# Kernel tuning notes

Measured on AMD Instinct MI355X. Metric: run time of the kernel, lower is better.

The kernel has to match this reference:

```python
import jax, jax.numpy as jnp
import numpy as np

NUM_LAYERS = 4  # -> 9 blocks: 4 encoder + bottleneck + 4 decoder
EPS = 1e-6
SQRT2 = float(np.sqrt(2.0))
INV_SQRT3 = float(1.0 / np.sqrt(3.0))


def _block(s, v, W0, W1, Wa, Wb):
    """_SelfInteractionUNet with full_square=False, irreps = Mx0e + Mx1o.

    tensor_square of per-channel (0e+1o):
      0e: s*s ; 0e: |v|^2/sqrt(3) ; 1o: sqrt(2)*s*v ; (2e is produced by e3nn
      but irreps_out has no 2e so the Linear discards it -> omitted here).
    """
    M = s.shape[-1]
    ts0a = s * s                                    # [N, M] 0e
    ts0b = jnp.sum(v * v, axis=-1) * INV_SQRT3      # [N, M] 0e
    ts1 = SQRT2 * s[..., None] * v                  # [N, M, 3] 1o
    s_in = jnp.concatenate([s, ts0a, ts0b], axis=-1)   # [N, 3M]
    v_in = jnp.concatenate([v, ts1], axis=1)           # [N, 2M, 3]
    # irreps-segmented Linear with path (fan-in) normalization
    s2 = (s_in @ W0) * (1.0 / np.sqrt(s_in.shape[-1]))               # [N, Mo]
    v2 = jnp.einsum('ncd,co->nod', v_in, W1) * (1.0 / np.sqrt(v_in.shape[1]))  # [N, Mo, 3]
    Mo = W0.shape[-1]
    # gated MLP on invariants (0e part), silu after each layer
    h = jax.nn.silu((s2 @ Wa) * (1.0 / np.sqrt(Mo)))                 # [N, Mo]
    g = jax.nn.silu((h @ Wb) * (1.0 / np.sqrt(Mo)))                  # [N, 2Mo]
    s2 = s2 * g[:, :Mo]
    v2 = v2 * g[:, Mo:, None]
    return s2, v2


def _eq_layernorm(s, v):
    # scalars: center + RMS normalize; vectors: norm-RMS normalize (equivariant)
    s = s - jnp.mean(s, axis=-1, keepdims=True)
    s = s * jax.lax.rsqrt(jnp.mean(s * s, axis=-1, keepdims=True) + EPS)
    v = v * jax.lax.rsqrt(jnp.mean(v * v, axis=(1, 2), keepdims=True) + EPS)
    return s, v


def _unet(scalars, vectors, W0, W1, Wa, Wb):
    s, v = scalars, vectors
    skips = []
    for i in range(NUM_LAYERS):
        s, v = _block(s, v, W0[i], W1[i], Wa[i], Wb[i])
        s, v = _eq_layernorm(s, v)
        skips.append((s, v))
    s, v = _block(s, v, W0[NUM_LAYERS], W1[NUM_LAYERS], Wa[NUM_LAYERS], Wb[NUM_LAYERS])
    for j in range(NUM_LAYERS):
        ss, vs = skips[NUM_LAYERS - 1 - j]
        s, v = s + ss, v + vs
        k = NUM_LAYERS + 1 + j
        s, v = _block(s, v, W0[k], W1[k], Wa[k], Wb[k])
        if j < NUM_LAYERS - 1:  # no norm on last decoder layer (norm_last=False)
            s, v = _eq_layernorm(s, v)
    N = s.shape[0]
    return jnp.concatenate([s, v.reshape(N, -1)], axis=-1)  # [N, 4M] irreps_array layout


def setup_inputs() -> dict:
    key = jax.random.key(0)
    ks = jax.random.split(key, 6)
    N, M = 16384, 256
    return {
        'scalars': jax.random.normal(ks[0], (N, M), jnp.float32),
        'vectors': jax.random.normal(ks[1], (N, M, 3), jnp.float32),
        'W0': jax.random.normal(ks[2], (9, 3 * M, M), jnp.float32),
        'W1': jax.random.normal(ks[3], (9, 2 * M, M), jnp.float32),
        'Wa': jax.random.normal(ks[4], (9, M, M), jnp.float32),
        'Wb': jax.random.normal(ks[5], (9, M, 2 * M), jnp.float32),
    }


def reference(scalars, vectors, W0, W1, Wa, Wb):
    return _unet(scalars, vectors, W0, W1, Wa, Wb)
```

## Files before the change

kernel.cpp:

```cpp
#include <hip/hip_runtime.h>
#include <hip/hip_bf16.h>
#include <math.h>


typedef __attribute__((ext_vector_type(8))) short bf16x8;
typedef __attribute__((ext_vector_type(4))) short bf16x4;
typedef __attribute__((ext_vector_type(4))) float f32x4;
typedef __attribute__((ext_vector_type(4))) _Float16 f16x4;

__device__ __forceinline__ unsigned asu(float f){ union{float f;unsigned u;}x; x.f=f; return x.u; }
__device__ __forceinline__ float asf(unsigned u){ union{unsigned u;float f;}x; x.u=u; return x.f; }

__device__ __forceinline__ unsigned short f2bf_r(float f){
  unsigned i = asu(f);
  return (unsigned short)((i + 0x7fffu + ((i >> 16) & 1u)) >> 16);
}
__device__ __forceinline__ float bf2f(unsigned short u){ return asf(((unsigned)u) << 16); }

__device__ __forceinline__ void split_t(float f, short& hi, short& lo){
  unsigned u = asu(f);
  hi = (short)(u >> 16);
  float lof = f - asf(u & 0xffff0000u);
  lo = (short)(asu(lof) >> 16);
}
__device__ __forceinline__ float rec(short h, short l){
  return asf(((unsigned)(unsigned short)h) << 16) + asf(((unsigned)(unsigned short)l) << 16);
}
__device__ __forceinline__ f32x4 rec4(const unsigned short* H, const unsigned short* L, size_t o){
  bf16x4 hv = *(const bf16x4*)(H + o);
  bf16x4 lv = *(const bf16x4*)(L + o);
  f32x4 f;
  #pragma unroll
  for (int j = 0; j < 4; ++j) f[j] = rec(hv[j], lv[j]);
  return f;
}

__global__ __launch_bounds__(256)
void transpose_w(const float* __restrict__ W, unsigned short* __restrict__ Wh,
                 unsigned short* __restrict__ Wl, int K, int Mo){
  __shared__ float tile[32][33];
  const int bi = blockIdx.z;
  const float* Wb = W + (size_t)bi * K * Mo;
  const size_t wo = (size_t)bi * K * Mo;
  const int k0 = blockIdx.x * 32, o0 = blockIdx.y * 32;
  const int tx = threadIdx.x & 31, ty = threadIdx.x >> 5;
  #pragma unroll
  for (int i = 0; i < 4; ++i){
    int k = ty + i * 8;
    tile[k][tx] = Wb[(size_t)(k0 + k) * Mo + o0 + tx];
  }
  __syncthreads();
  #pragma unroll
  for (int i = 0; i < 4; ++i){
    int o = ty + i * 8;
    float f = tile[tx][o];
    unsigned short h = f2bf_r(f);
    unsigned short l = f2bf_r(f - bf2f(h));
    Wh[wo + (size_t)(o0 + o) * K + k0 + tx] = h;
    Wl[wo + (size_t)(o0 + o) * K + k0 + tx] = l;
  }
}

__global__ __launch_bounds__(256)
void convert_inputs(const float* __restrict__ s, const float* __restrict__ v,
                    unsigned short* __restrict__ stH, unsigned short* __restrict__ stL,
                    int NM){
  int i = blockIdx.x * 256 + threadIdx.x;
  if (i >= NM) return;
  short h, l;
  split_t(s[i], h, l); stH[i] = h; stL[i] = l;
  const float* vp = v + (size_t)i * 3;
  #pragma unroll
  for (int d = 0; d < 3; ++d){
    split_t(vp[d], h, l);
    stH[(size_t)(1 + d) * NM + i] = h;
    stL[(size_t)(1 + d) * NM + i] = l;
  }
}

__global__ __launch_bounds__(256, 3)
void gemm_sv(const unsigned short* __restrict__ StH, const unsigned short* __restrict__ StL,
             const _Float16* __restrict__ skip,
             const unsigned short* __restrict__ W0h, const unsigned short* __restrict__ W0l,
             const unsigned short* __restrict__ W1h, const unsigned short* __restrict__ W1l,
             unsigned short* __restrict__ s2H, unsigned short* __restrict__ s2L,
             unsigned short* __restrict__ v2H, unsigned short* __restrict__ v2L,
             int NM, float cs, float cv)
{
  __shared__ unsigned short Ah[32][40], Al[32][40];
  __shared__ unsigned short Bhs[256][40], Bls[256][40];
  const int tid  = threadIdx.x;
  const int lane = tid & 63;
  const int wave = tid >> 6;
  const int wn   = wave * 64;
  const int row0 = blockIdx.x * 32;
  const int z    = blockIdx.z;
  const bool isS = (z == 0);
  const int dv   = z - 1;
  const int K    = isS ? 768 : 512;
  const float scale = isS ? cs : cv;
  const unsigned short* Bh = isS ? W0h : W1h;
  const unsigned short* Bl = isS ? W0l : W1l;
  unsigned short* outH = isS ? s2H : v2H + (size_t)dv * NM;
  unsigned short* outL = isS ? s2L : v2L + (size_t)dv * NM;
  const bool sk = (skip != nullptr);

  f32x4 acc[2][4];
  #pragma unroll
  for (int m = 0; m < 2; ++m)
    #pragma unroll
    for (int n = 0; n < 4; ++n) acc[m][n] = (f32x4){0.f,0.f,0.f,0.f};

  const int ar = tid >> 3;
  const int ac4 = (tid & 7) * 4;

  for (int k0 = 0; k0 < K; k0 += 32){
    const int seg = k0 >> 8;
    {
      const int gr = row0 + ar;
      const int c  = (k0 + ac4) & 255;
      const size_t o = (size_t)gr * 256 + c;
      if (!sk && seg == 0){
        const int p = isS ? 0 : 1 + dv;
        *(bf16x4*)(&Ah[ar][ac4]) = *(const bf16x4*)(StH + (size_t)p * NM + o);
        *(bf16x4*)(&Al[ar][ac4]) = *(const bf16x4*)(StL + (size_t)p * NM + o);
      } else {
        f32x4 f;
        if (isS){
          if (seg <= 1){
            f32x4 x = rec4(StH, StL, o);
            if (sk){
              f16x4 y = *(const f16x4*)(skip + o);
              #pragma unroll
              for (int j = 0; j < 4; ++j) x[j] += (float)y[j];
            }
            if (seg == 0){
              f = x;
            } else {
              #pragma unroll
              for (int j = 0; j < 4; ++j) f[j] = x[j]*x[j];
            }
          } else {
            f32x4 a0 = rec4(StH, StL, (size_t)NM + o);
            f32x4 a1 = rec4(StH, StL, (size_t)2*NM + o);
            f32x4 a2 = rec4(StH, StL, (size_t)3*NM + o);
            if (sk){
              f16x4 b0 = *(const f16x4*)(skip + (size_t)NM + o);
              f16x4 b1 = *(const f16x4*)(skip + (size_t)2*NM + o);
              f16x4 b2 = *(const f16x4*)(skip + (size_t)3*NM + o);
              #pragma unroll
              for (int j = 0; j < 4; ++j){ a0[j]+=(float)b0[j]; a1[j]+=(float)b1[j]; a2[j]+=(float)b2[j]; }
            }
            #pragma unroll
            for (int j = 0; j < 4; ++j)
              f[j] = (a0[j]*a0[j] + a1[j]*a1[j] + a2[j]*a2[j]) * 0.57735026918962576f;
          }
        } else {
          f32x4 x = rec4(StH, StL, (size_t)(1+dv)*NM + o);
          if (sk){
            f16x4 y = *(const f16x4*)(skip + (size_t)(1+dv)*NM + o);
            #pragma unroll
            for (int j = 0; j < 4; ++j) x[j] += (float)y[j];
          }
          if (seg == 0){
            f = x;
          } else {
            f32x4 s = rec4(StH, StL, o);
            if (sk){
              f16x4 y = *(const f16x4*)(skip + o);
              #pragma unroll
              for (int j = 0; j < 4; ++j) s[j] += (float)y[j];
            }
            #pragma unroll
            for (int j = 0; j < 4; ++j) f[j] = 1.41421356237309505f * s[j] * x[j];
          }
        }
        bf16x4 hi, lo;
        #pragma unroll
        for (int j = 0; j < 4; ++j){ short h, l; split_t(f[j], h, l); hi[j]=h; lo[j]=l; }
        *(bf16x4*)(&Ah[ar][ac4]) = hi;
        *(bf16x4*)(&Al[ar][ac4]) = lo;
      }
    }
    #pragma unroll
    for (int it = 0; it < 4; ++it){
      int idx = tid + it * 256;
      int br  = idx >> 2;
      int kc  = (idx & 3) * 8;
      const size_t o = (size_t)br * K + k0 + kc;
      *(bf16x8*)(&Bhs[br][kc]) = *(const bf16x8*)(Bh + o);
      *(bf16x8*)(&Bls[br][kc]) = *(const bf16x8*)(Bl + o);
    }
    __syncthreads();

    const int arow = lane & 15;
    const int kq   = (lane >> 4) * 8;
    bf16x8 ah[2], al[2], bh[4], bl[4];
    #pragma unroll
    for (int m = 0; m < 2; ++m){
      ah[m] = *(const bf16x8*)(&Ah[m*16 + arow][kq]);
      al[m] = *(const bf16x8*)(&Al[m*16 + arow][kq]);
    }
    #pragma unroll
    for (int n = 0; n < 4; ++n){
      bh[n] = *(const bf16x8*)(&Bhs[wn + n*16 + arow][kq]);
      bl[n] = *(const bf16x8*)(&Bls[wn + n*16 + arow][kq]);
    }
    #pragma unroll
    for (int m = 0; m < 2; ++m)
      #pragma unroll
      for (int n = 0; n < 4; ++n){
        acc[m][n] = __builtin_amdgcn_mfma_f32_16x16x32_bf16(ah[m], bh[n], acc[m][n], 0, 0, 0);
        acc[m][n] = __builtin_amdgcn_mfma_f32_16x16x32_bf16(al[m], bh[n], acc[m][n], 0, 0, 0);
        acc[m][n] = __builtin_amdgcn_mfma_f32_16x16x32_bf16(ah[m], bl[n], acc[m][n], 0, 0, 0);
      }
    __syncthreads();
  }

  #pragma unroll
  for (int m = 0; m < 2; ++m){
    #pragma unroll
    for (int n = 0; n < 4; ++n){
      const int cg = wn + n * 16 + (lane & 15);
      #pragma unroll
      for (int j = 0; j < 4; ++j){
        const int rg = row0 + m * 16 + ((lane >> 4) * 4) + j;
        short h, l; split_t(acc[m][n][j] * scale, h, l);
        outH[(size_t)rg * 256 + cg] = (unsigned short)h;
        outL[(size_t)rg * 256 + cg] = (unsigned short)l;
      }
    }
  }
}

template<int EPI>
__global__ __launch_bounds__(256, 3)
void gemm_hg(const unsigned short* __restrict__ AhG, const unsigned short* __restrict__ AlG,
             const unsigned short* __restrict__ Bh, const unsigned short* __restrict__ Bl,
             int NM, float scale,
             unsigned short* __restrict__ outH, unsigned short* __restrict__ outL,
             const unsigned short* __restrict__ s2H, const unsigned short* __restrict__ s2L,
             const unsigned short* __restrict__ v2H, const unsigned short* __restrict__ v2L,
             unsigned short* __restrict__ stH, unsigned short* __restrict__ stL,
             float* __restrict__ fout)
{
  __shared__ unsigned short Ah[32][40], Al[32][40];
  __shared__ unsigned short Bhs[256][40], Bls[256][40];
  const int tid  = threadIdx.x;
  const int lane = tid & 63;
  const int wave = tid >> 6;
  const int wn   = wave * 64;
  const int row0 = blockIdx.x * 32;
  const int col0 = blockIdx.y * 256;
  const int K = 256;

  f32x4 acc[2][4];
  #pragma unroll
  for (int m = 0; m < 2; ++m)
    #pragma unroll
    for (int n = 0; n < 4; ++n) acc[m][n] = (f32x4){0.f,0.f,0.f,0.f};

  const int ar = tid >> 3;
  const int ac4 = (tid & 7) * 4;

  for (int k0 = 0; k0 < K; k0 += 32){
    {
      const size_t o = (size_t)(row0 + ar) * 256 + k0 + ac4;
      *(bf16x4*)(&Ah[ar][ac4]) = *(const bf16x4*)(AhG + o);
      *(bf16x4*)(&Al[ar][ac4]) = *(const bf16x4*)(AlG + o);
    }
    #pragma unroll
    for (int it = 0; it < 4; ++it){
      int idx = tid + it * 256;
      int br  = idx >> 2;
      int kc  = (idx & 3) * 8;
      const size_t o = (size_t)(col0 + br) * K + k0 + kc;
      *(bf16x8*)(&Bhs[br][kc]) = *(const bf16x8*)(Bh + o);
      *(bf16x8*)(&Bls[br][kc]) = *(const bf16x8*)(Bl + o);
    }
    __syncthreads();

    const int arow = lane & 15;
    const int kq   = (lane >> 4) * 8;
    bf16x8 ah[2], al[2], bh[4], bl[4];
    #pragma unroll
    for (int m = 0; m < 2; ++m){
      ah[m] = *(const bf16x8*)(&Ah[m*16 + arow][kq]);
      al[m] = *(const bf16x8*)(&Al[m*16 + arow][kq]);
    }
    #pragma unroll
    for (int n = 0; n < 4; ++n){
      bh[n] = *(const bf16x8*)(&Bhs[wn + n*16 + arow][kq]);
      bl[n] = *(const bf16x8*)(&Bls[wn + n*16 + arow][kq]);
    }
    #pragma unroll
    for (int m = 0; m < 2; ++m)
      #pragma unroll
      for (int n = 0; n < 4; ++n){
        acc[m][n] = __builtin_amdgcn_mfma_f32_16x16x32_bf16(ah[m], bh[n], acc[m][n], 0, 0, 0);
        acc[m][n] = __builtin_amdgcn_mfma_f32_16x16x32_bf16(al[m], bh[n], acc[m][n], 0, 0, 0);
        acc[m][n] = __builtin_amdgcn_mfma_f32_16x16x32_bf16(ah[m], bl[n], acc[m][n], 0, 0, 0);
      }
    __syncthreads();
  }

  #pragma unroll
  for (int m = 0; m < 2; ++m){
    #pragma unroll
    for (int n = 0; n < 4; ++n){
      const int cl = wn + n * 16 + (lane & 15);
      const int cg = col0 + cl;
      #pragma unroll
      for (int j = 0; j < 4; ++j){
        const int rg = row0 + m * 16 + ((lane >> 4) * 4) + j;
        float val = acc[m][n][j] * scale;
        if (EPI == 1){
          float sl = val / (1.f + expf(-val));
          short h, l; split_t(sl, h, l);
          outH[(size_t)rg * 256 + cg] = (unsigned short)h;
          outL[(size_t)rg * 256 + cg] = (unsigned short)l;
        } else {
          float gv = val / (1.f + expf(-val));
          if (cg < 256){
            const size_t o = (size_t)rg * 256 + cg;
            float sval = rec(s2H[o], s2L[o]) * gv;
            if (EPI == 2){
              short h, l; split_t(sval, h, l);
              stH[o] = (unsigned short)h; stL[o] = (unsigned short)l;
            } else {
              fout[(size_t)rg * 1024 + cg] = sval;
            }
          } else {
            const int c = cg - 256;
            #pragma unroll
            for (int d = 0; d < 3; ++d){
              const size_t o = (size_t)d * NM + (size_t)rg * 256 + c;
              float vv = rec(v2H[o], v2L[o]) * gv;
              if (EPI == 2){
                short h, l; split_t(vv, h, l);
                stH[(size_t)(1+d) * NM + (size_t)rg * 256 + c] = (unsigned short)h;
                stL[(size_t)(1+d) * NM + (size_t)rg * 256 + c] = (unsigned short)l;
              } else {
                fout[(size_t)rg * 1024 + 256 + 3 * (size_t)c + d] = vv;
              }
            }
          }
        }
      }
    }
  }
}

__global__ __launch_bounds__(256)
void ln_k(unsigned short* __restrict__ stH, unsigned short* __restrict__ stL,
          _Float16* __restrict__ snap, int NM){
  const int row  = blockIdx.x * 4 + (threadIdx.x >> 6);
  const int lane = threadIdx.x & 63;
  const size_t o = (size_t)row * 256 + lane * 4;
  f32x4 sv = rec4(stH, stL, o);
  f32x4 v0 = rec4(stH, stL, (size_t)NM + o);
  f32x4 v1 = rec4(stH, stL, (size_t)2*NM + o);
  f32x4 v2 = rec4(stH, stL, (size_t)3*NM + o);
  float r0 = 0.f, r1 = 0.f, r2 = 0.f;
  #pragma unroll
  for (int j = 0; j < 4; ++j){
    r0 += sv[j];
    r1 += sv[j] * sv[j];
    r2 += v0[j]*v0[j] + v1[j]*v1[j] + v2[j]*v2[j];
  }
  #pragma unroll
  for (int off = 1; off < 64; off <<= 1){
    r0 += __shfl_xor(r0, off, 64);
    r1 += __shfl_xor(r1, off, 64);
    r2 += __shfl_xor(r2, off, 64);
  }
  float mu  = r0 * (1.f / 256.f);
  float var = r1 * (1.f / 256.f) - mu * mu;
  float srs = rsqrtf(var + 1e-6f);
  float vrs = rsqrtf(r2 * (1.f / 768.f) + 1e-6f);
  f32x4 pl[4];
  #pragma unroll
  for (int j = 0; j < 4; ++j){
    pl[0][j] = (sv[j] - mu) * srs;
    pl[1][j] = v0[j] * vrs; pl[2][j] = v1[j] * vrs; pl[3][j] = v2[j] * vrs;
  }
  #pragma unroll
  for (int p = 0; p < 4; ++p){
    bf16x4 hv, lv; f16x4 hx;
    #pragma unroll
    for (int j = 0; j < 4; ++j){
      short h, l; split_t(pl[p][j], h, l);
      hv[j] = h; lv[j] = l; hx[j] = (_Float16)pl[p][j];
    }
    *(bf16x4*)(stH + (size_t)p*NM + o) = hv;
    *(bf16x4*)(stL + (size_t)p*NM + o) = lv;
    if (snap) *(f16x4*)(snap + (size_t)p*NM + o) = hx;
  }
}

extern "C" void kernel_launch(void* const* d_in, const int* in_sizes, int n_in,
                              void* d_out, int out_size, void* d_ws, size_t ws_size,
                              hipStream_t stream){
  const float* s_in = (const float*)d_in[0];
  const float* v_in = (const float*)d_in[1];
  const float* W0 = (const float*)d_in[2];
  const float* W1 = (const float*)d_in[3];
  const float* Wa = (const float*)d_in[4];
  const float* Wb = (const float*)d_in[5];
  const int Mdim = 256;
  const int N  = in_sizes[0] / Mdim;
  const int NM = N * Mdim;

  unsigned short* ws = (unsigned short*)d_ws;
  size_t off = 0;
  auto alloc = [&](size_t elems){ unsigned short* p = ws + off; off += elems; return p; };
  unsigned short* W0h = alloc((size_t)9 * 768 * 256);
  unsigned short* W0l = alloc((size_t)9 * 768 * 256);
  unsigned short* W1h = alloc((size_t)9 * 512 * 256);
  unsigned short* W1l = alloc((size_t)9 * 512 * 256);
  unsigned short* Wah = alloc((size_t)9 * 256 * 256);
  unsigned short* Wal = alloc((size_t)9 * 256 * 256);
  unsigned short* Wbh = alloc((size_t)9 * 256 * 512);
  unsigned short* Wbl = alloc((size_t)9 * 256 * 512);
  unsigned short* s2H = alloc(NM);
  unsigned short* s2L = alloc(NM);
  unsigned short* v2H = alloc((size_t)3 * NM);
  unsigned short* v2L = alloc((size_t)3 * NM);
  unsigned short* hH  = alloc(NM);
  unsigned short* hL  = alloc(NM);
  _Float16* skips = (_Float16*)(ws + off);
  (void)ws_size;

  unsigned short* stateH = (unsigned short*)d_out;
  unsigned short* stateL = stateH + (size_t)4 * NM;

  dim3 blk(256);
  transpose_w<<<dim3(768/32, 256/32, 9), blk, 0, stream>>>(W0, W0h, W0l, 768, 256);
  transpose_w<<<dim3(512/32, 256/32, 9), blk, 0, stream>>>(W1, W1h, W1l, 512, 256);
  transpose_w<<<dim3(256/32, 256/32, 9), blk, 0, stream>>>(Wa, Wah, Wal, 256, 256);
  transpose_w<<<dim3(256/32, 512/32, 9), blk, 0, stream>>>(Wb, Wbh, Wbl, 256, 512);
  convert_inputs<<<dim3(NM/256), blk, 0, stream>>>(s_in, v_in, stateH, stateL, NM);

  const float c_s2 = 1.f / sqrtf(768.f);
  const float c_v2 = 1.f / sqrtf(512.f);
  const float c_hg = 1.f / 16.f;
  const int gx = N / 32;

  auto run_block = [&](int i, const _Float16* skip, bool fin){
    const unsigned short* w0h = W0h + (size_t)i * 768 * 256;
    const unsigned short* w0l = W0l + (size_t)i * 768 * 256;
    const unsigned short* w1h = W1h + (size_t)i * 512 * 256;
    const unsigned short* w1l = W1l + (size_t)i * 512 * 256;
    const unsigned short* wah = Wah + (size_t)i * 256 * 256;
    const unsigned short* wal = Wal + (size_t)i * 256 * 256;
    const unsigned short* wbh = Wbh + (size_t)i * 256 * 512;
    const unsigned short* wbl = Wbl + (size_t)i * 256 * 512;
    gemm_sv<<<dim3(gx, 1, 4), blk, 0, stream>>>(stateH, stateL, skip,
                                                w0h, w0l, w1h, w1l,
                                                s2H, s2L, v2H, v2L, NM, c_s2, c_v2);
    gemm_hg<1><<<dim3(gx, 1), blk, 0, stream>>>(s2H, s2L, wah, wal, NM, c_hg,
                                                hH, hL, nullptr, nullptr, nullptr, nullptr,
                                                nullptr, nullptr, nullptr);
    if (!fin)
      gemm_hg<2><<<dim3(gx, 2), blk, 0, stream>>>(hH, hL, wbh, wbl, NM, c_hg,
                                                  nullptr, nullptr, s2H, s2L, v2H, v2L,
                                                  stateH, stateL, nullptr);
    else
      gemm_hg<3><<<dim3(gx, 2), blk, 0, stream>>>(hH, hL, wbh, wbl, NM, c_hg,
                                                  nullptr, nullptr, s2H, s2L, v2H, v2L,
                                                  nullptr, nullptr, (float*)d_out);
  };

  for (int i = 0; i < 4; ++i){
    run_block(i, nullptr, false);
    ln_k<<<dim3(N/4), blk, 0, stream>>>(stateH, stateL, skips + (size_t)i * 4 * NM, NM);
  }
  run_block(4, nullptr, false);
  for (int j = 0; j < 4; ++j){
    run_block(5 + j, skips + (size_t)(3 - j) * 4 * NM, j == 3);
    if (j < 3) ln_k<<<dim3(N/4), blk, 0, stream>>>(stateH, stateL, nullptr, NM);
  }
}
```

Before: 2.152 ms.

## Retile split-bf16 GEMMs to 128x128 blocks with 512 threads and swizzled LDS

Both GEMM kernels move from 32-row x 256-column tiles with 256 threads to 128x128 tiles with 8 waves (4x2 wave grid) and a K-step of 64. Shared memory switches from padded rows to an XOR-swizzled layout to avoid LDS bank conflicts. The larger square tile reuses A rows across more columns and cuts redundant weight reloads per output. The cost is a 64 KB LDS footprint per block, fewer blocks overall, and higher register pressure under launch bounds of 512 threads with 4 blocks per CU.

```diff
diff --git a/kernel.cpp b/kernel.cpp
--- a/kernel.cpp
+++ b/kernel.cpp
@@ -33,6 +33,10 @@
   #pragma unroll
   for (int j = 0; j < 4; ++j) f[j] = rec(hv[j], lv[j]);
   return f;
+}
+
+__device__ __forceinline__ int LO(int r, int kc){
+  return r * 64 + ((((kc >> 3) ^ (r & 7)) << 3) | (kc & 7));
 }
 
 __global__ __launch_bounds__(256)
@@ -78,7 +82,7 @@
   }
 }
 
-__global__ __launch_bounds__(256, 3)
+__global__ __launch_bounds__(512, 4)
 void gemm_sv(const unsigned short* __restrict__ StH, const unsigned short* __restrict__ StL,
              const _Float16* __restrict__ skip,
              const unsigned short* __restrict__ W0h, const unsigned short* __restrict__ W0l,
@@ -87,144 +91,174 @@
              unsigned short* __restrict__ v2H, unsigned short* __restrict__ v2L,
              int NM, float cs, float cv)
 {
-  __shared__ unsigned short Ah[32][40], Al[32][40];
-  __shared__ unsigned short Bhs[256][40], Bls[256][40];
-  const int tid  = threadIdx.x;
-  const int lane = tid & 63;
-  const int wave = tid >> 6;
-  const int wn   = wave * 64;
-  const int row0 = blockIdx.x * 32;
-  const int z    = blockIdx.z;
-  const bool isS = (z == 0);
-  const int dv   = z - 1;
-  const int K    = isS ? 768 : 512;
+  __shared__ unsigned short Ash[128*64], Asl[128*64], Bsh[128*64], Bsl[128*64];
+  const int tid = threadIdx.x;
+  const int lane = tid & 63, wave = tid >> 6;
+  const int wm = (wave >> 1) * 32, wn = (wave & 1) * 64;
+  const int row0 = blockIdx.x * 128;
+  const int z = blockIdx.y;
+  const bool isS = (z < 2);
+  const int dv = (z - 2) >> 1;
+  const int col0 = isS ? z * 128 : ((z - 2) & 1) * 128;
+  const int K = isS ? 768 : 512;
   const float scale = isS ? cs : cv;
-  const unsigned short* Bh = isS ? W0h : W1h;
-  const unsigned short* Bl = isS ? W0l : W1l;
+  const unsigned short* Bhg = isS ? W0h : W1h;
+  const unsigned short* Blg = isS ? W0l : W1l;
   unsigned short* outH = isS ? s2H : v2H + (size_t)dv * NM;
   unsigned short* outL = isS ? s2L : v2L + (size_t)dv * NM;
   const bool sk = (skip != nullptr);
 
   f32x4 acc[2][4];
   #pragma unroll
-  for (int m = 0; m < 2; ++m)
+  for (int m = 0; m < 2; ++m){
     #pragma unroll
     for (int n = 0; n < 4; ++n) acc[m][n] = (f32x4){0.f,0.f,0.f,0.f};
-
-  const int ar = tid >> 3;
-  const int ac4 = (tid & 7) * 4;
-
-  for (int k0 = 0; k0 < K; k0 += 32){
-    const int seg = k0 >> 8;
+  }
+
+  const int bc = tid >> 2, bk = (tid & 3) * 16;
+  const int arr = bc, akc = bk;
+
+  for (int k0 = 0; k0 < K; k0 += 64){
     {
-      const int gr = row0 + ar;
-      const int c  = (k0 + ac4) & 255;
+      const size_t o = (size_t)(col0 + bc) * K + k0 + bk;
+      bf16x8 x0 = *(const bf16x8*)(Bhg + o);
+      bf16x8 x1 = *(const bf16x8*)(Bhg + o + 8);
+      bf16x8 y0 = *(const bf16x8*)(Blg + o);
+      bf16x8 y1 = *(const bf16x8*)(Blg + o + 8);
+      *(bf16x8*)(&Bsh[LO(bc, bk)])     = x0;
+      *(bf16x8*)(&Bsh[LO(bc, bk + 8)]) = x1;
+      *(bf16x8*)(&Bsl[LO(bc, bk)])     = y0;
+      *(bf16x8*)(&Bsl[LO(bc, bk + 8)]) = y1;
+    }
+    {
+      const int gr = row0 + arr;
+      const int c  = (k0 + akc) & 255;
       const size_t o = (size_t)gr * 256 + c;
+      const int seg = k0 >> 8;
       if (!sk && seg == 0){
         const int p = isS ? 0 : 1 + dv;
-        *(bf16x4*)(&Ah[ar][ac4]) = *(const bf16x4*)(StH + (size_t)p * NM + o);
-        *(bf16x4*)(&Al[ar][ac4]) = *(const bf16x4*)(StL + (size_t)p * NM + o);
+        const unsigned short* SH = StH + (size_t)p * NM;
+        const unsigned short* SL = StL + (size_t)p * NM;
+        *(bf16x8*)(&Ash[LO(arr, akc)])     = *(const bf16x8*)(SH + o);
+        *(bf16x8*)(&Ash[LO(arr, akc + 8)]) = *(const bf16x8*)(SH + o + 8);
+        *(bf16x8*)(&Asl[LO(arr, akc)])     = *(const bf16x8*)(SL + o);
+        *(bf16x8*)(&Asl[LO(arr, akc + 8)]) = *(const bf16x8*)(SL + o + 8);
       } else {
-        f32x4 f;
+        f32x4 f[4];
         if (isS){
           if (seg <= 1){
-            f32x4 x = rec4(StH, StL, o);
+            #pragma unroll
+            for (int q = 0; q < 4; ++q){
+              f32x4 x = rec4(StH, StL, o + 4*q);
+              if (sk){
+                f16x4 y = *(const f16x4*)(skip + o + 4*q);
+                #pragma unroll
+                for (int j = 0; j < 4; ++j) x[j] += (float)y[j];
+              }
+              if (seg == 0){
+                f[q] = x;
+              } else {
+                #pragma unroll
+                for (int j = 0; j < 4; ++j) f[q][j] = x[j] * x[j];
+              }
+            }
+          } else {
+            #pragma unroll
+            for (int q = 0; q < 4; ++q){
+              f32x4 a0 = rec4(StH, StL, (size_t)NM + o + 4*q);
+              f32x4 a1 = rec4(StH, StL, (size_t)2*NM + o + 4*q);
+              f32x4 a2 = rec4(StH, StL, (size_t)3*NM + o + 4*q);
+              if (sk){
+                f16x4 b0 = *(const f16x4*)(skip + (size_t)NM + o + 4*q);
+                f16x4 b1 = *(const f16x4*)(skip + (size_t)2*NM + o + 4*q);
+                f16x4 b2 = *(const f16x4*)(skip + (size_t)3*NM + o + 4*q);
+                #pragma unroll
+                for (int j = 0; j < 4; ++j){
+                  a0[j] += (float)b0[j]; a1[j] += (float)b1[j]; a2[j] += (float)b2[j];
+                }
+              }
+              #pragma unroll
+              for (int j = 0; j < 4; ++j)
+                f[q][j] = (a0[j]*a0[j] + a1[j]*a1[j] + a2[j]*a2[j]) * 0.57735026918962576f;
+            }
+          }
+        } else {
+          #pragma unroll
+          for (int q = 0; q < 4; ++q){
+            f32x4 x = rec4(StH, StL, (size_t)(1 + dv)*NM + o + 4*q);
             if (sk){
-              f16x4 y = *(const f16x4*)(skip + o);
+              f16x4 y = *(const f16x4*)(skip + (size_t)(1 + dv)*NM + o + 4*q);
               #pragma unroll
               for (int j = 0; j < 4; ++j) x[j] += (float)y[j];
             }
             if (seg == 0){
-              f = x;
+              f[q] = x;
             } else {
+              f32x4 s = rec4(StH, StL, o + 4*q);
+              if (sk){
+                f16x4 y = *(const f16x4*)(skip + o + 4*q);
+                #pragma unroll
+                for (int j = 0; j < 4; ++j) s[j] += (float)y[j];
+              }
               #pragma unroll
-              for (int j = 0; j < 4; ++j) f[j] = x[j]*x[j];
+              for (int j = 0; j < 4; ++j) f[q][j] = 1.41421356237309505f * s[j] * x[j];
             }
-          } else {
-            f32x4 a0 = rec4(StH, StL, (size_t)NM + o);
-            f32x4 a1 = rec4(StH, StL, (size_t)2*NM + o);
-            f32x4 a2 = rec4(StH, StL, (size_t)3*NM + o);
-            if (sk){
-              f16x4 b0 = *(const f16x4*)(skip + (size_t)NM + o);
-              f16x4 b1 = *(const f16x4*)(skip + (size_t)2*NM + o);
-              f16x4 b2 = *(const f16x4*)(skip + (size_t)3*NM + o);
-              #pragma unroll
-              for (int j = 0; j < 4; ++j){ a0[j]+=(float)b0[j]; a1[j]+=(float)b1[j]; a2[j]+=(float)b2[j]; }
-            }
-            #pragma unroll
-            for (int j = 0; j < 4; ++j)
-              f[j] = (a0[j]*a0[j] + a1[j]*a1[j] + a2[j]*a2[j]) * 0.57735026918962576f;
-          }
-        } else {
-          f32x4 x = rec4(StH, StL, (size_t)(1+dv)*NM + o);
-          if (sk){
-            f16x4 y = *(const f16x4*)(skip + (size_t)(1+dv)*NM + o);
-            #pragma unroll
-            for (int j = 0; j < 4; ++j) x[j] += (float)y[j];
-          }
-          if (seg == 0){
-            f = x;
-          } else {
-            f32x4 s = rec4(StH, StL, o);
-            if (sk){
-              f16x4 y = *(const f16x4*)(skip + o);
-              #pragma unroll
-              for (int j = 0; j < 4; ++j) s[j] += (float)y[j];
-            }
-            #pragma unroll
-            for (int j = 0; j < 4; ++j) f[j] = 1.41421356237309505f * s[j] * x[j];
           }
         }
-        bf16x4 hi, lo;
         #pragma unroll
-        for (int j = 0; j < 4; ++j){ short h, l; split_t(f[j], h, l); hi[j]=h; lo[j]=l; }
-        *(bf16x4*)(&Ah[ar][ac4]) = hi;
-        *(bf16x4*)(&Al[ar][ac4]) = lo;
-      }
-    }
-    #pragma unroll
-    for (int it = 0; it < 4; ++it){
-      int idx = tid + it * 256;
-      int br  = idx >> 2;
-      int kc  = (idx & 3) * 8;
-      const size_t o = (size_t)br * K + k0 + kc;
-      *(bf16x8*)(&Bhs[br][kc]) = *(const bf16x8*)(Bh + o);
-      *(bf16x8*)(&Bls[br][kc]) = *(const bf16x8*)(Bl + o);
+        for (int q = 0; q < 2; ++q){
+          bf16x8 hi, lo;
+          #pragma unroll
+          for (int j = 0; j < 8; ++j){
+            short h, l; split_t(f[q*2 + (j >> 2)][j & 3], h, l);
+            hi[j] = h; lo[j] = l;
+          }
+          *(bf16x8*)(&Ash[LO(arr, akc + q*8)]) = hi;
+          *(bf16x8*)(&Asl[LO(arr, akc + q*8)]) = lo;
+        }
+      }
     }
     __syncthreads();
 
     const int arow = lane & 15;
-    const int kq   = (lane >> 4) * 8;
-    bf16x8 ah[2], al[2], bh[4], bl[4];
-    #pragma unroll
-    for (int m = 0; m < 2; ++m){
-      ah[m] = *(const bf16x8*)(&Ah[m*16 + arow][kq]);
-      al[m] = *(const bf16x8*)(&Al[m*16 + arow][kq]);
-    }
+    const int ksl  = (lane >> 4) * 8;
+    #pragma unroll
+    for (int ks = 0; ks < 2; ++ks){
+      const int kq = ks * 32 + ksl;
+      bf16x8 ah[2], al[2], bh[4], bl[4];
+      #pragma unroll
+      for (int m = 0; m < 2; ++m){
+        const int r = wm + m*16 + arow;
+        ah[m] = *(const bf16x8*)(&Ash[LO(r, kq)]);
+        al[m] = *(const bf16x8*)(&Asl[LO(r, kq)]);
+      }
+      #pragma unroll
+      for (int n = 0; n < 4; ++n){
+        const int r = wn + n*16 + arow;
+        bh[n] = *(const bf16x8*)(&Bsh[LO(r, kq)]);
+        bl[n] = *(const bf16x8*)(&Bsl[LO(r, kq)]);
+      }
+      #pragma unroll
+      for (int m = 0; m < 2; ++m){
+        #pragma unroll
+        for (int n = 0; n < 4; ++n){
+          acc[m][n] = __builtin_amdgcn_mfma_f32_16x16x32_bf16(ah[m], bh[n], acc[m][n], 0, 0, 0);
+          acc[m][n] = __builtin_amdgcn_mfma_f32_16x16x32_bf16(al[m], bh[n], acc[m][n], 0, 0, 0);
+          acc[m][n] = __builtin_amdgcn_mfma_f32_16x16x32_bf16(ah[m], bl[n], acc[m][n], 0, 0, 0);
+        }
+      }
+    }
+    __syncthreads();
+  }
+
+  #pragma unroll
+  for (int m = 0; m < 2; ++m){
     #pragma unroll
     for (int n = 0; n < 4; ++n){
-      bh[n] = *(const bf16x8*)(&Bhs[wn + n*16 + arow][kq]);
-      bl[n] = *(const bf16x8*)(&Bls[wn + n*16 + arow][kq]);
-    }
-    #pragma unroll
-    for (int m = 0; m < 2; ++m)
-      #pragma unroll
-      for (int n = 0; n < 4; ++n){
-        acc[m][n] = __builtin_amdgcn_mfma_f32_16x16x32_bf16(ah[m], bh[n], acc[m][n], 0, 0, 0);
-        acc[m][n] = __builtin_amdgcn_mfma_f32_16x16x32_bf16(al[m], bh[n], acc[m][n], 0, 0, 0);
-        acc[m][n] = __builtin_amdgcn_mfma_f32_16x16x32_bf16(ah[m], bl[n], acc[m][n], 0, 0, 0);
-      }
-    __syncthreads();
-  }
-
-  #pragma unroll
-  for (int m = 0; m < 2; ++m){
-    #pragma unroll
-    for (int n = 0; n < 4; ++n){
-      const int cg = wn + n * 16 + (lane & 15);
+      const int cg = col0 + wn + n*16 + (lane & 15);
       #pragma unroll
       for (int j = 0; j < 4; ++j){
-        const int rg = row0 + m * 16 + ((lane >> 4) * 4) + j;
+        const int rg = row0 + wm + m*16 + ((lane >> 4) * 4) + j;
         short h, l; split_t(acc[m][n][j] * scale, h, l);
         outH[(size_t)rg * 256 + cg] = (unsigned short)h;
         outL[(size_t)rg * 256 + cg] = (unsigned short)l;
@@ -234,7 +268,7 @@
 }
 
 template<int EPI>
-__global__ __launch_bounds__(256, 3)
+__global__ __launch_bounds__(512, 4)
 void gemm_hg(const unsigned short* __restrict__ AhG, const unsigned short* __restrict__ AlG,
              const unsigned short* __restrict__ Bh, const unsigned short* __restrict__ Bl,
              int NM, float scale,
@@ -244,75 +278,83 @@
              unsigned short* __restrict__ stH, unsigned short* __restrict__ stL,
              float* __restrict__ fout)
 {
-  __shared__ unsigned short Ah[32][40], Al[32][40];
-  __shared__ unsigned short Bhs[256][40], Bls[256][40];
-  const int tid  = threadIdx.x;
-  const int lane = tid & 63;
-  const int wave = tid >> 6;
-  const int wn   = wave * 64;
-  const int row0 = blockIdx.x * 32;
-  const int col0 = blockIdx.y * 256;
+  __shared__ unsigned short Ash[128*64], Asl[128*64], Bsh[128*64], Bsl[128*64];
+  const int tid = threadIdx.x;
+  const int lane = tid & 63, wave = tid >> 6;
+  const int wm = (wave >> 1) * 32, wn = (wave & 1) * 64;
+  const int row0 = blockIdx.x * 128;
+  const int col0 = blockIdx.y * 128;
   const int K = 256;
 
   f32x4 acc[2][4];
   #pragma unroll
-  for (int m = 0; m < 2; ++m)
+  for (int m = 0; m < 2; ++m){
     #pragma unroll
     for (int n = 0; n < 4; ++n) acc[m][n] = (f32x4){0.f,0.f,0.f,0.f};
-
-  const int ar = tid >> 3;
-  const int ac4 = (tid & 7) * 4;
-
-  for (int k0 = 0; k0 < K; k0 += 32){
+  }
+
+  const int bc = tid >> 2, bk = (tid & 3) * 16;
+
+  for (int k0 = 0; k0 < K; k0 += 64){
     {
-      const size_t o = (size_t)(row0 + ar) * 256 + k0 + ac4;
-      *(bf16x4*)(&Ah[ar][ac4]) = *(const bf16x4*)(AhG + o);
-      *(bf16x4*)(&Al[ar][ac4]) = *(const bf16x4*)(AlG + o);
-    }
-    #pragma unroll
-    for (int it = 0; it < 4; ++it){
-      int idx = tid + it * 256;
-      int br  = idx >> 2;
-      int kc  = (idx & 3) * 8;
-      const size_t o = (size_t)(col0 + br) * K + k0 + kc;
-      *(bf16x8*)(&Bhs[br][kc]) = *(const bf16x8*)(Bh + o);
-      *(bf16x8*)(&Bls[br][kc]) = *(const bf16x8*)(Bl + o);
+      const size_t o = (size_t)(col0 + bc) * K + k0 + bk;
+      bf16x8 x0 = *(const bf16x8*)(Bh + o);
+      bf16x8 x1 = *(const bf16x8*)(Bh + o + 8);
+      bf16x8 y0 = *(const bf16x8*)(Bl + o);
+      bf16x8 y1 = *(const bf16x8*)(Bl + o + 8);
+      *(bf16x8*)(&Bsh[LO(bc, bk)])     = x0;
+      *(bf16x8*)(&Bsh[LO(bc, bk + 8)]) = x1;
+      *(bf16x8*)(&Bsl[LO(bc, bk)])     = y0;
+      *(bf16x8*)(&Bsl[LO(bc, bk + 8)]) = y1;
+    }
+    {
+      const size_t o = (size_t)(row0 + bc) * 256 + k0 + bk;
+      *(bf16x8*)(&Ash[LO(bc, bk)])     = *(const bf16x8*)(AhG + o);
+      *(bf16x8*)(&Ash[LO(bc, bk + 8)]) = *(const bf16x8*)(AhG + o + 8);
+      *(bf16x8*)(&Asl[LO(bc, bk)])     = *(const bf16x8*)(AlG + o);
+      *(bf16x8*)(&Asl[LO(bc, bk + 8)]) = *(const bf16x8*)(AlG + o + 8);
     }
     __syncthreads();
 
     const int arow = lane & 15;
-    const int kq   = (lane >> 4) * 8;
-    bf16x8 ah[2], al[2], bh[4], bl[4];
-    #pragma unroll
-    for (int m = 0; m < 2; ++m){
-      ah[m] = *(const bf16x8*)(&Ah[m*16 + arow][kq]);
-      al[m] = *(const bf16x8*)(&Al[m*16 + arow][kq]);
-    }
+    const int ksl  = (lane >> 4) * 8;
+    #pragma unroll
+    for (int ks = 0; ks < 2; ++ks){
+      const int kq = ks * 32 + ksl;
+      bf16x8 ah[2], al[2], bh[4], bl[4];
+      #pragma unroll
+      for (int m = 0; m < 2; ++m){
+        const int r = wm + m*16 + arow;
+        ah[m] = *(const bf16x8*)(&Ash[LO(r, kq)]);
+        al[m] = *(const bf16x8*)(&Asl[LO(r, kq)]);
+      }
+      #pragma unroll
+      for (int n = 0; n < 4; ++n){
+        const int r = wn + n*16 + arow;
+        bh[n] = *(const bf16x8*)(&Bsh[LO(r, kq)]);
+        bl[n] = *(const bf16x8*)(&Bsl[LO(r, kq)]);
+      }
+      #pragma unroll
+      for (int m = 0; m < 2; ++m){
+        #pragma unroll
+        for (int n = 0; n < 4; ++n){
+          acc[m][n] = __builtin_amdgcn_mfma_f32_16x16x32_bf16(ah[m], bh[n], acc[m][n], 0, 0, 0);
+          acc[m][n] = __builtin_amdgcn_mfma_f32_16x16x32_bf16(al[m], bh[n], acc[m][n], 0, 0, 0);
+          acc[m][n] = __builtin_amdgcn_mfma_f32_16x16x32_bf16(ah[m], bl[n], acc[m][n], 0, 0, 0);
+        }
+      }
+    }
+    __syncthreads();
+  }
+
+  #pragma unroll
+  for (int m = 0; m < 2; ++m){
     #pragma unroll
     for (int n = 0; n < 4; ++n){
-      bh[n] = *(const bf16x8*)(&Bhs[wn + n*16 + arow][kq]);
-      bl[n] = *(const bf16x8*)(&Bls[wn + n*16 + arow][kq]);
-    }
-    #pragma unroll
-    for (int m = 0; m < 2; ++m)
-      #pragma unroll
-      for (int n = 0; n < 4; ++n){
-        acc[m][n] = __builtin_amdgcn_mfma_f32_16x16x32_bf16(ah[m], bh[n], acc[m][n], 0, 0, 0);
-        acc[m][n] = __builtin_amdgcn_mfma_f32_16x16x32_bf16(al[m], bh[n], acc[m][n], 0, 0, 0);
-        acc[m][n] = __builtin_amdgcn_mfma_f32_16x16x32_bf16(ah[m], bl[n], acc[m][n], 0, 0, 0);
-      }
-    __syncthreads();
-  }
-
-  #pragma unroll
-  for (int m = 0; m < 2; ++m){
-    #pragma unroll
-    for (int n = 0; n < 4; ++n){
-      const int cl = wn + n * 16 + (lane & 15);
-      const int cg = col0 + cl;
+      const int cg = col0 + wn + n*16 + (lane & 15);
       #pragma unroll
       for (int j = 0; j < 4; ++j){
-        const int rg = row0 + m * 16 + ((lane >> 4) * 4) + j;
+        const int rg = row0 + wm + m*16 + ((lane >> 4) * 4) + j;
         float val = acc[m][n][j] * scale;
         if (EPI == 1){
           float sl = val / (1.f + expf(-val));
@@ -435,6 +477,7 @@
   unsigned short* stateL = stateH + (size_t)4 * NM;
 
   dim3 blk(256);
+  dim3 blk5(512);
   transpose_w<<<dim3(768/32, 256/32, 9), blk, 0, stream>>>(W0, W0h, W0l, 768, 256);
   transpose_w<<<dim3(512/32, 256/32, 9), blk, 0, stream>>>(W1, W1h, W1l, 512, 256);
   transpose_w<<<dim3(256/32, 256/32, 9), blk, 0, stream>>>(Wa, Wah, Wal, 256, 256);
@@ -444,7 +487,7 @@
   const float c_s2 = 1.f / sqrtf(768.f);
   const float c_v2 = 1.f / sqrtf(512.f);
   const float c_hg = 1.f / 16.f;
-  const int gx = N / 32;
+  const int gx = N / 128;
 
   auto run_block = [&](int i, const _Float16* skip, bool fin){
     const unsigned short* w0h = W0h + (size_t)i * 768 * 256;
@@ -455,20 +498,20 @@
     const unsigned short* wal = Wal + (size_t)i * 256 * 256;
     const unsigned short* wbh = Wbh + (size_t)i * 256 * 512;
     const unsigned short* wbl = Wbl + (size_t)i * 256 * 512;
-    gemm_sv<<<dim3(gx, 1, 4), blk, 0, stream>>>(stateH, stateL, skip,
-                                                w0h, w0l, w1h, w1l,
-                                                s2H, s2L, v2H, v2L, NM, c_s2, c_v2);
-    gemm_hg<1><<<dim3(gx, 1), blk, 0, stream>>>(s2H, s2L, wah, wal, NM, c_hg,
-                                                hH, hL, nullptr, nullptr, nullptr, nullptr,
-                                                nullptr, nullptr, nullptr);
+    gemm_sv<<<dim3(gx, 8), blk5, 0, stream>>>(stateH, stateL, skip,
+                                              w0h, w0l, w1h, w1l,
+                                              s2H, s2L, v2H, v2L, NM, c_s2, c_v2);
+    gemm_hg<1><<<dim3(gx, 2), blk5, 0, stream>>>(s2H, s2L, wah, wal, NM, c_hg,
+                                                 hH, hL, nullptr, nullptr, nullptr, nullptr,
+                                                 nullptr, nullptr, nullptr);
     if (!fin)
-      gemm_hg<2><<<dim3(gx, 2), blk, 0, stream>>>(hH, hL, wbh, wbl, NM, c_hg,
-                                                  nullptr, nullptr, s2H, s2L, v2H, v2L,
-                                                  stateH, stateL, nullptr);
+      gemm_hg<2><<<dim3(gx, 4), blk5, 0, stream>>>(hH, hL, wbh, wbl, NM, c_hg,
+                                                   nullptr, nullptr, s2H, s2L, v2H, v2L,
+                                                   stateH, stateL, nullptr);
     else
-      gemm_hg<3><<<dim3(gx, 2), blk, 0, stream>>>(hH, hL, wbh, wbl, NM, c_hg,
-                                                  nullptr, nullptr, s2H, s2L, v2H, v2L,
-                                                  nullptr, nullptr, (float*)d_out);
+      gemm_hg<3><<<dim3(gx, 4), blk5, 0, stream>>>(hH, hL, wbh, wbl, NM, c_hg,
+                                                   nullptr, nullptr, s2H, s2L, v2H, v2L,
+                                                   nullptr, nullptr, (float*)d_out);
   };
 
   for (int i = 0; i < 4; ++i){
```

Measured after the change: 2.043 ms. 1.05x faster.
